# Performance work log

Hardware: AMD Instinct MI355X
Metric: run time of the kernel (lower is better)

Reference implementation:

```python
import jax, jax.numpy as jnp
import numpy as np

B, N, K, DEG = 512, 128, 8, 16
NR = 200            # num_rels (padding idx = NR)
INP, SEM, EMB, L = 32, 16, 32, 3
FEAT = INP - SEM
NN = B * N
E = NN * DEG
OUT = L * EMB       # 96


def _gru_cell(x, h, Wih, Whh, bih, bhh):
    gi = x @ Wih.T + bih
    gh = h @ Whh.T + bhh
    ir, iz, i_n = jnp.split(gi, 3, axis=-1)
    hr, hz, hn = jnp.split(gh, 3, axis=-1)
    r = jax.nn.sigmoid(ir + hr)
    z = jax.nn.sigmoid(iz + hz)
    n = jnp.tanh(i_n + r * hn)
    return (1.0 - z) * n + z * h


def _run_gru(xs, h0, Wih, Whh, bih, bhh):
    # xs: [T, batch, in]
    def step(h, x):
        h2 = _gru_cell(x, h, Wih, Whh, bih, bhh)
        return h2, h2
    hT, ys = jax.lax.scan(step, h0, xs)
    return ys, hT


def _forward(feat, out_nei_rels, in_nei_rels, r_label_node, src, dst, etype, rel_labels,
             rel_emb, w_rel2ent_W, w_rel2ent_b, W_msg, W_self, b_gnn, W_rel,
             gru_bias, gru_Wih_f, gru_Whh_f, gru_bih_f, gru_bhh_f,
             gru_Wih_b, gru_Whh_b, gru_bih_b, gru_bhh_b,
             Wo_W, Wo_b, path_Wih, path_Whh, path_bih, path_bhh, fc_W, fc_b):
    # --- init_ent_emb_matrix: neighbor-relation attention vs target relation ---
    out_e = rel_emb[out_nei_rels]                      # [NN,K,INP]
    in_e = rel_emb[in_nei_rels]                        # [NN,K,INP]
    tgt = rel_emb[r_label_node]                        # [NN,INP]
    out_att = jax.nn.softmax(jnp.einsum('nkd,nd->nk', out_e, tgt), axis=1)
    in_att = jax.nn.softmax(jnp.einsum('nkd,nd->nk', in_e, tgt), axis=1)
    out_sem = jnp.einsum('nk,nkd->nd', out_att, out_e)
    in_sem = jnp.einsum('nk,nkd->nd', in_att, in_e)
    sem = jax.nn.sigmoid(jnp.concatenate([out_sem, in_sem], axis=1) @ w_rel2ent_W + w_rel2ent_b)
    h = jnp.concatenate([feat, sem], axis=1)           # [NN,INP]

    # --- RGCN-style relational message passing; repr = concat of layer outputs ---
    r = rel_emb
    deg = jnp.maximum(jax.ops.segment_sum(jnp.ones((E,), h.dtype), dst, NN), 1.0)[:, None]
    reprs = []
    for l in range(L):
        msg = h[src] * r[etype]                        # [E,EMB]  (gather-heavy)
        agg = jax.ops.segment_sum(msg, dst, NN) / deg  # mean aggregation
        h = jax.nn.relu(agg @ W_msg[l] + h @ W_self[l] + b_gnn[l])
        r = r @ W_rel[l]                               # relation stream (padding row stays 0)
        reprs.append(h)
    repr_ = jnp.concatenate(reprs, axis=1)             # [NN,OUT]
    r_emb_out = r                                      # [NR+1,EMB]

    # --- BatchGRU: bidirectional GRU over each graph's node sequence ---
    node = repr_.reshape(B, N, OUT)
    message = jax.nn.relu(node + gru_bias)
    h0 = jnp.max(node, axis=1)                         # per-graph max init hidden
    xs = jnp.swapaxes(message, 0, 1)                   # [N,B,OUT]
    ys_f, _ = _run_gru(xs, h0, gru_Wih_f, gru_Whh_f, gru_bih_f, gru_bhh_f)
    ys_b, _ = _run_gru(xs[::-1], h0, gru_Wih_b, gru_Whh_b, gru_bih_b, gru_bhh_b)
    gru_out = jnp.concatenate([ys_f, ys_b[::-1]], axis=-1)  # [N,B,2*OUT]
    repr2 = jax.nn.relu(jnp.swapaxes(gru_out, 0, 1).reshape(NN, 2 * OUT))
    node_hidden = jax.nn.relu(repr2 @ Wo_W + Wo_b)     # [NN,OUT]

    nh = node_hidden.reshape(B, N, OUT)
    g_out = jnp.mean(nh, axis=1)                       # mean_nodes
    head_embs = nh[:, 0]                               # node id==1 is node 0 of each graph
    tail_embs = nh[:, 1]                               # node id==2 is node 1 of each graph

    # --- nei_rel_path: GRU over (h_r, r_t, t_r) triples, attention aggregation ---
    in_rels = in_nei_rels.reshape(B, N, K)
    heads_rels = in_rels[:, 0]                         # [B,K]
    tails_rels = in_rels[:, 1]                         # [B,K]
    P = K * K
    paths = jnp.stack([
        jnp.repeat(heads_rels, K, axis=1),
        jnp.broadcast_to(rel_labels[:, None], (B, P)),
        jnp.tile(tails_rels, (1, K)),
    ], axis=-1).reshape(B * P, 3)
    pe = r_emb_out[paths]                              # [B*P,3,EMB]
    _, last = _run_gru(jnp.swapaxes(pe, 0, 1), jnp.zeros((B * P, EMB), pe.dtype),
                       path_Wih, path_Whh, path_bih, path_bhh)
    last = last.reshape(B, P, EMB)
    r_lab_e = r_emb_out[rel_labels]                    # [B,EMB]
    atts = jax.nn.softmax(jnp.einsum('bpe,be->bp', last, r_lab_e), axis=1)
    g_p = jnp.einsum('bp,bpe->be', atts, last)         # [B,EMB]

    g_rep = jnp.concatenate([g_out, head_embs, tail_embs, r_lab_e, g_p], axis=1)  # [B,352]
    return g_rep @ fc_W + fc_b                         # [B,1]


def setup_inputs():
    key = jax.random.key(0)
    ks = jax.random.split(key, 40)
    idx = iter(range(40))
    def nk():
        return ks[next(idx)]
    def _p(shape, scale=0.1):
        return jax.random.normal(nk(), shape, jnp.float32) * scale

    feat = jax.random.normal(nk(), (NN, FEAT), jnp.float32)
    out_nei_rels = jax.random.randint(nk(), (NN, K), 0, NR)
    in_nei_rels = jax.random.randint(nk(), (NN, K), 0, NR)
    rel_labels = jax.random.randint(nk(), (B,), 0, NR)
    r_label_node = jnp.repeat(rel_labels, N)
    gid = jnp.arange(E) // (N * DEG)                   # edges stay within their graph
    src = gid * N + jax.random.randint(nk(), (E,), 0, N)
    dst = gid * N + jax.random.randint(nk(), (E,), 0, N)
    etype = jax.random.randint(nk(), (E,), 0, NR)
    rel_emb = jax.random.normal(nk(), (NR + 1, INP), jnp.float32) * 0.5
    rel_emb = rel_emb.at[NR].set(0.0)                  # padding_idx row

    return {
        'feat': feat, 'out_nei_rels': out_nei_rels, 'in_nei_rels': in_nei_rels,
        'r_label_node': r_label_node, 'src': src, 'dst': dst, 'etype': etype,
        'rel_labels': rel_labels, 'rel_emb': rel_emb,
        'w_rel2ent_W': _p((2 * INP, SEM)), 'w_rel2ent_b': _p((SEM,)),
        'W_msg': _p((L, EMB, EMB)), 'W_self': _p((L, EMB, EMB)),
        'b_gnn': _p((L, EMB)), 'W_rel': _p((L, INP, INP)),
        'gru_bias': _p((OUT,)),
        'gru_Wih_f': _p((3 * OUT, OUT)), 'gru_Whh_f': _p((3 * OUT, OUT)),
        'gru_bih_f': _p((3 * OUT,)), 'gru_bhh_f': _p((3 * OUT,)),
        'gru_Wih_b': _p((3 * OUT, OUT)), 'gru_Whh_b': _p((3 * OUT, OUT)),
        'gru_bih_b': _p((3 * OUT,)), 'gru_bhh_b': _p((3 * OUT,)),
        'Wo_W': _p((2 * OUT, OUT)), 'Wo_b': _p((OUT,)),
        'path_Wih': _p((3 * EMB, EMB)), 'path_Whh': _p((3 * EMB, EMB)),
        'path_bih': _p((3 * EMB,)), 'path_bhh': _p((3 * EMB,)),
        'fc_W': _p((3 * OUT + 2 * EMB, 1)), 'fc_b': _p((1,)),
    }


def reference(feat, out_nei_rels, in_nei_rels, r_label_node, src, dst, etype, rel_labels,
              rel_emb, w_rel2ent_W, w_rel2ent_b, W_msg, W_self, b_gnn, W_rel,
              gru_bias, gru_Wih_f, gru_Whh_f, gru_bih_f, gru_bhh_f,
              gru_Wih_b, gru_Whh_b, gru_bih_b, gru_bhh_b,
              Wo_W, Wo_b, path_Wih, path_Whh, path_bih, path_bhh, fc_W, fc_b):
    return _forward(feat, out_nei_rels, in_nei_rels, r_label_node, src, dst, etype, rel_labels,
                    rel_emb, w_rel2ent_W, w_rel2ent_b, W_msg, W_self, b_gnn, W_rel,
                    gru_bias, gru_Wih_f, gru_Whh_f, gru_bih_f, gru_bhh_f,
                    gru_Wih_b, gru_Whh_b, gru_bih_b, gru_bhh_b,
                    Wo_W, Wo_b, path_Wih, path_Whh, path_bih, path_bhh, fc_W, fc_b)
```

## Files before the change

### kernel.cpp

```cpp
#include <hip/hip_runtime.h>
#include <math.h>

#define BB 512
#define NT 128
#define NREL 201
#define NNODE (BB*NT)
#define NEDGE (NNODE*16)

typedef float f32x4 __attribute__((ext_vector_type(4)));
typedef __attribute__((ext_vector_type(8))) short bf16x8;

__device__ __forceinline__ float sigm(float x) { return 1.f/(1.f + __expf(-x)); }

__device__ __forceinline__ unsigned short f2bf(float f) {
  unsigned u; __builtin_memcpy(&u, &f, 4);
  unsigned r = u + 0x7fffu + ((u >> 16) & 1u);
  return (unsigned short)(r >> 16);
}

__global__ __launch_bounds__(96) void k_rel2(const float* __restrict__ rel_emb,
                                             const float* __restrict__ W_rel,
                                             const float* __restrict__ pWih,
                                             const float* __restrict__ pbih,
                                             float* __restrict__ r123,
                                             float* __restrict__ XI) {
  __shared__ float ra[32], rb[32];
  int r = blockIdx.x, tid = threadIdx.x;
  if (tid < 32) ra[tid] = rel_emb[r*32 + tid];
  __syncthreads();
  if (tid < 32) {
    float s = 0.f;
    #pragma unroll
    for (int d = 0; d < 32; ++d) s += ra[d]*W_rel[d*32 + tid];
    rb[tid] = s; r123[0*NREL*32 + r*32 + tid] = s;
  }
  __syncthreads();
  if (tid < 32) {
    float s = 0.f;
    #pragma unroll
    for (int d = 0; d < 32; ++d) s += rb[d]*W_rel[1024 + d*32 + tid];
    ra[tid] = s; r123[1*NREL*32 + r*32 + tid] = s;
  }
  __syncthreads();
  if (tid < 32) {
    float s = 0.f;
    #pragma unroll
    for (int d = 0; d < 32; ++d) s += ra[d]*W_rel[2048 + d*32 + tid];
    rb[tid] = s; r123[2*NREL*32 + r*32 + tid] = s;
  }
  __syncthreads();
  float s = pbih[tid];
  #pragma unroll
  for (int d = 0; d < 32; ++d) s += rb[d]*pWih[tid*32 + d];
  XI[r*96 + tid] = s;
}

__global__ __launch_bounds__(256) void k_wt1(const float* __restrict__ Wih_f,
                                             const float* __restrict__ Wih_b,
                                             const float* __restrict__ bih_f,
                                             const float* __restrict__ bih_b,
                                             const float* __restrict__ Wo_W,
                                             unsigned short* __restrict__ WT1bt,
                                             unsigned short* __restrict__ WoBt,
                                             float* __restrict__ bcat) {
  int i = blockIdx.x*256 + threadIdx.x;
  if (i < 576*96) {
    int j = i / 96;
    float v = (j < 288) ? Wih_f[i] : Wih_b[i - 288*96];
    WT1bt[i] = f2bf(v);
  }
  if (i < 96*192) {
    int j = i / 192, k = i - j*192;
    WoBt[i] = f2bf(Wo_W[k*96 + j]);
  }
  if (i < 576) bcat[i] = (i < 288) ? bih_f[i] : bih_b[i-288];
}

__device__ __forceinline__ void sem_att(const float* __restrict__ rel_emb,
                                        const int rels[8], const float tgt[32],
                                        float out[32]) {
  float dots[8]; float mx = -1e30f;
  #pragma unroll
  for (int k = 0; k < 8; ++k) {
    const float4* er = (const float4*)(rel_emb + rels[k]*32);
    float s = 0.f;
    #pragma unroll
    for (int q = 0; q < 8; ++q) {
      float4 v = er[q];
      s += v.x*tgt[4*q+0] + v.y*tgt[4*q+1] + v.z*tgt[4*q+2] + v.w*tgt[4*q+3];
    }
    dots[k] = s; mx = fmaxf(mx, s);
  }
  float den = 0.f;
  #pragma unroll
  for (int k = 0; k < 8; ++k) { float e = __expf(dots[k]-mx); dots[k] = e; den += e; }
  float inv = 1.f/den;
  #pragma unroll
  for (int d = 0; d < 32; ++d) out[d] = 0.f;
  #pragma unroll
  for (int k = 0; k < 8; ++k) {
    const float4* er = (const float4*)(rel_emb + rels[k]*32);
    float a = dots[k]*inv;
    #pragma unroll
    for (int q = 0; q < 8; ++q) {
      float4 v = er[q];
      out[4*q+0] += a*v.x; out[4*q+1] += a*v.y; out[4*q+2] += a*v.z; out[4*q+3] += a*v.w;
    }
  }
}

__global__ __launch_bounds__(256) void k_sem(
    const float* __restrict__ feat, const int* __restrict__ out_rels,
    const int* __restrict__ in_rels, const int* __restrict__ r_label_node,
    const float* __restrict__ rel_emb, const float* __restrict__ W,
    const float* __restrict__ bias, float* __restrict__ hin) {
  int n = blockIdx.x*256 + threadIdx.x;
  float tgt[32];
  {
    const float4* tr = (const float4*)(rel_emb + r_label_node[n]*32);
    #pragma unroll
    for (int q = 0; q < 8; ++q) {
      float4 v = tr[q];
      tgt[4*q+0]=v.x; tgt[4*q+1]=v.y; tgt[4*q+2]=v.z; tgt[4*q+3]=v.w;
    }
  }
  int ro[8], ri[8];
  #pragma unroll
  for (int k = 0; k < 8; ++k) { ro[k] = out_rels[n*8+k]; ri[k] = in_rels[n*8+k]; }
  float osem[32], isem[32];
  sem_att(rel_emb, ro, tgt, osem);
  sem_att(rel_emb, ri, tgt, isem);
  const float4* fr = (const float4*)(feat + (size_t)n*16);
  float4* ho = (float4*)(hin + (size_t)n*32);
  #pragma unroll
  for (int q = 0; q < 4; ++q) ho[q] = fr[q];
  #pragma unroll
  for (int j = 0; j < 16; ++j) {
    float s = bias[j];
    #pragma unroll
    for (int d = 0; d < 32; ++d) s += osem[d]*W[d*16+j] + isem[d]*W[(32+d)*16+j];
    hin[(size_t)n*32 + 16 + j] = sigm(s);
  }
}

__global__ __launch_bounds__(512) void k_gnn3(
    const float* __restrict__ hin, const float* __restrict__ rel_emb,
    const float* __restrict__ r123,
    const int* __restrict__ src, const int* __restrict__ dst, const int* __restrict__ etype,
    const float* __restrict__ W_msg, const float* __restrict__ W_self,
    const float* __restrict__ b_gnn,
    float* __restrict__ AT, float* __restrict__ ghid0) {
  __shared__ __align__(16) float hl[NT*36];
  __shared__ __align__(16) float hnew[NT*33];
  __shared__ float rl[NREL*32];
  __shared__ unsigned short eidx[2048];
  __shared__ float scratch[16][32];
  __shared__ int cnt[128], fill[128], scanv[128], rowstart[129];
  int g = blockIdx.x;
  int tid = threadIdx.x;
  int d = tid & 31, grp = tid >> 5;

  for (int i = tid; i < NT*32; i += 512) {
    int row = i >> 5, col = i & 31;
    hl[row*36 + col] = hin[(size_t)(g*NT + row)*32 + col];
  }
  if (tid < 128) { cnt[tid] = 0; fill[tid] = 0; }
  __syncthreads();
  for (int i = tid; i < 2048; i += 512)
    atomicAdd(&cnt[dst[g*2048 + i] - g*NT], 1);
  __syncthreads();
  if (tid < 128) scanv[tid] = cnt[tid];
  __syncthreads();
  #pragma unroll
  for (int off = 1; off < 128; off <<= 1) {
    int v = 0;
    if (tid < 128 && tid >= off) v = scanv[tid - off];
    __syncthreads();
    if (tid < 128) scanv[tid] += v;
    __syncthreads();
  }
  if (tid < 128) { rowstart[tid+1] = scanv[tid]; if (tid == 0) rowstart[0] = 0; }
  __syncthreads();
  for (int i = tid; i < 2048; i += 512) {
    int e = g*2048 + i;
    int dl = dst[e] - g*NT;
    int slot = rowstart[dl] + atomicAdd(&fill[dl], 1);
    eidx[slot] = (unsigned short)(((src[e] - g*NT) << 8) | etype[e]);
  }

  for (int l = 0; l < 3; ++l) {
    const float* rsrc = (l == 0) ? rel_emb : (r123 + (size_t)(l-1)*NREL*32);
    for (int i = tid; i < NREL*32; i += 512) rl[i] = rsrc[i];
    float wm[32], ws[32];
    #pragma unroll
    for (int dd = 0; dd < 32; ++dd) {
      wm[dd] = W_msg[l*1024 + dd*32 + d];
      ws[dd] = W_self[l*1024 + dd*32 + d];
    }
    float bj = b_gnn[l*32 + d];
    __syncthreads();
    for (int k2 = 0; k2 < 8; ++k2) {
      int n = grp + k2*16;
      int e0 = rowstart[n], e1 = rowstart[n+1];
      float acc = 0.f;
      for (int e = e0; e < e1; ++e) {
        int pk = eidx[e];
        acc += hl[(pk >> 8)*36 + d] * rl[(pk & 255)*32 + d];
      }
      scratch[grp][d] = acc;
      float invd = 1.f / (float)((e1 - e0) > 0 ? (e1 - e0) : 1);
      float sa = 0.f, sh = 0.f;
      #pragma unroll
      for (int dd = 0; dd < 32; ++dd) {
        sa += scratch[grp][dd]*wm[dd];
        sh += hl[n*36 + dd]*ws[dd];
      }
      hnew[n*33 + d] = fmaxf(bj + invd*sa + sh, 0.f);
    }
    __syncthreads();
    for (int i = tid; i < NT*32; i += 512) {
      int row = i >> 5, col = i & 31;
      hl[row*36 + col] = hnew[row*33 + col];
    }
    #pragma unroll
    for (int pass = 0; pass < 8; ++pass) {
      int col = (pass << 2) + (tid >> 7);
      int row = tid & 127;
      AT[(size_t)(l*32 + col)*NNODE + g*NT + row] = hnew[row*33 + col];
    }
    {
      float m = -1e30f;
      #pragma unroll
      for (int k2 = 0; k2 < 8; ++k2) m = fmaxf(m, hnew[(grp + k2*16)*33 + d]);
      scratch[grp][d] = m;
    }
    __syncthreads();
    if (tid < 32) {
      float m = -1e30f;
      #pragma unroll
      for (int p2 = 0; p2 < 16; ++p2) m = fmaxf(m, scratch[p2][tid]);
      ghid0[g*96 + l*32 + tid] = m;
    }
    __syncthreads();
  }
}

__global__ __launch_bounds__(256) void k_gemm1m(
    const float* __restrict__ AT, const float* __restrict__ gbias,
    const unsigned short* __restrict__ WT1bt, const float* __restrict__ bcat,
    float* __restrict__ GI) {
  __shared__ unsigned short As[128*104];
  int m0 = blockIdx.x * 128;
  int tid = threadIdx.x;
  for (int i = tid; i < 96*32; i += 256) {
    int r = i >> 5, c4 = i & 31;
    float4 v = *(const float4*)&AT[(size_t)r*NNODE + m0 + c4*4];
    float b = gbias[r];
    As[(c4*4+0)*104 + r] = f2bf(fmaxf(v.x+b,0.f));
    As[(c4*4+1)*104 + r] = f2bf(fmaxf(v.y+b,0.f));
    As[(c4*4+2)*104 + r] = f2bf(fmaxf(v.z+b,0.f));
    As[(c4*4+3)*104 + r] = f2bf(fmaxf(v.w+b,0.f));
  }
  __syncthreads();
  int w = tid >> 6, l = tid & 63;
  int lr = l & 15, lh = l >> 4;
  bf16x8 afr[2][3];
  #pragma unroll
  for (int tm = 0; tm < 2; ++tm)
    #pragma unroll
    for (int kc = 0; kc < 3; ++kc)
      afr[tm][kc] = *(const bf16x8*)&As[((w*2+tm)*16 + lr)*104 + kc*32 + lh*8];
  for (int nb = 0; nb < 9; ++nb) {
    int n0 = nb*64;
    #pragma unroll
    for (int tn = 0; tn < 4; ++tn) {
      int col = n0 + tn*16 + lr;
      const unsigned short* bp = WT1bt + (size_t)col*96 + lh*8;
      bf16x8 b0 = *(const bf16x8*)(bp);
      bf16x8 b1 = *(const bf16x8*)(bp + 32);
      bf16x8 b2 = *(const bf16x8*)(bp + 64);
      float bb = bcat[col];
      #pragma unroll
      for (int tm = 0; tm < 2; ++tm) {
        f32x4 acc = {bb, bb, bb, bb};
        acc = __builtin_amdgcn_mfma_f32_16x16x32_bf16(afr[tm][0], b0, acc, 0, 0, 0);
        acc = __builtin_amdgcn_mfma_f32_16x16x32_bf16(afr[tm][1], b1, acc, 0, 0, 0);
        acc = __builtin_amdgcn_mfma_f32_16x16x32_bf16(afr[tm][2], b2, acc, 0, 0, 0);
        int rbase = m0 + (w*2+tm)*16 + lh*4;
        #pragma unroll
        for (int r = 0; r < 4; ++r)
          __builtin_nontemporal_store(acc[r], &GI[(size_t)(rbase + r)*576 + col]);
      }
    }
  }
}

#define PIN4(v) asm volatile("" : "+v"(v.x), "+v"(v.y), "+v"(v.z), "+v"(v.w))
#define DOT16(acc, W0,W1,W2,W3, X0,X1,X2,X3) \
  acc += W0.x*X0.x + W0.y*X0.y + W0.z*X0.z + W0.w*X0.w \
       + W1.x*X1.x + W1.y*X1.y + W1.z*X1.z + W1.w*X1.w \
       + W2.x*X2.x + W2.y*X2.y + W2.z*X2.z + W2.w*X2.w \
       + W3.x*X3.x + W3.y*X3.y + W3.z*X3.z + W3.w*X3.w

__global__ __launch_bounds__(576, 1) void k_gru(
    const float* __restrict__ Whh_f, const float* __restrict__ bhh_f,
    const float* __restrict__ Whh_b, const float* __restrict__ bhh_b,
    const float* __restrict__ GI, const float* __restrict__ ghid0,
    float* __restrict__ AT2) {
  __shared__ __align__(16) float h_lds[4][96];
  __shared__ float part[4][288][9];
  int bx = blockIdx.x;
  int dir = bx >> 7;
  int gbase = (bx & 127) * 4;
  int tid = threadIdx.x;
  int c = tid % 96;
  int p = tid / 96;
  bool fin = (tid < 384);
  int s = p;

  const float* Whh = dir ? Whh_b : Whh_f;
  const float4* wr0 = (const float4*)(Whh + (size_t)c*96 + p*16);
  const float4* wr1 = (const float4*)(Whh + (size_t)(96+c)*96 + p*16);
  const float4* wr2 = (const float4*)(Whh + (size_t)(192+c)*96 + p*16);
  float4 wa0=wr0[0], wa1=wr0[1], wa2=wr0[2], wa3=wr0[3];
  float4 wb0=wr1[0], wb1=wr1[1], wb2=wr1[2], wb3=wr1[3];
  float4 wc0=wr2[0], wc1=wr2[1], wc2=wr2[2], wc3=wr2[3];

  float bh0=0.f, bh1=0.f, bh2=0.f;
  float gi0=0.f, gi1=0.f, gi2=0.f;
  if (fin) {
    const float* bhh = dir ? bhh_b : bhh_f;
    bh0 = bhh[c]; bh1 = bhh[96+c]; bh2 = bhh[192+c];
    h_lds[s][c] = ghid0[(gbase+s)*96 + c];
    int pos0 = dir ? 127 : 0;
    const float* g = GI + (size_t)((gbase+s)*128 + pos0)*576 + dir*288;
    gi0 = g[c]; gi1 = g[96+c]; gi2 = g[192+c];
  }
  __syncthreads();
  for (int t = 0; t < 128; ++t) {
    PIN4(wa0); PIN4(wa1); PIN4(wa2); PIN4(wa3);
    PIN4(wb0); PIN4(wb1); PIN4(wb2); PIN4(wb3);
    PIN4(wc0); PIN4(wc1); PIN4(wc2); PIN4(wc3);
    int pos = dir ? (127-t) : t;
    float gn0=0.f, gn1=0.f, gn2=0.f;
    if (fin && t < 127) {
      int posn = dir ? (126-t) : (t+1);
      const float* g = GI + (size_t)((gbase+s)*128 + posn)*576 + dir*288;
      gn0 = g[c]; gn1 = g[96+c]; gn2 = g[192+c];
    }
    #pragma unroll
    for (int s4 = 0; s4 < 4; ++s4) {
      const float4* hh = (const float4*)&h_lds[s4][p*16];
      float4 x0=hh[0], x1=hh[1], x2=hh[2], x3=hh[3];
      float q0=0.f, q1=0.f, q2=0.f;
      DOT16(q0, wa0,wa1,wa2,wa3, x0,x1,x2,x3);
      DOT16(q1, wb0,wb1,wb2,wb3, x0,x1,x2,x3);
      DOT16(q2, wc0,wc1,wc2,wc3, x0,x1,x2,x3);
      part[s4][c][p]     = q0;
      part[s4][96+c][p]  = q1;
      part[s4][192+c][p] = q2;
    }
    __syncthreads();
    if (fin) {
      const float* pr = part[s][c];
      const float* pz = part[s][96+c];
      const float* pn = part[s][192+c];
      float ghr = pr[0]+pr[1]+pr[2]+pr[3]+pr[4]+pr[5] + bh0;
      float ghz = pz[0]+pz[1]+pz[2]+pz[3]+pz[4]+pz[5] + bh1;
      float ghn = pn[0]+pn[1]+pn[2]+pn[3]+pn[4]+pn[5] + bh2;
      float r  = sigm(gi0 + ghr);
      float z  = sigm(gi1 + ghz);
      float nn = tanhf(gi2 + r*ghn);
      float hv = (1.f - z)*nn + z*h_lds[s][c];
      h_lds[s][c] = hv;
      AT2[(size_t)(dir*96 + c)*NNODE + (gbase+s)*128 + pos] = fmaxf(hv, 0.f);
      gi0 = gn0; gi1 = gn1; gi2 = gn2;
    }
    __syncthreads();
  }
}

__global__ __launch_bounds__(384) void k_gemm2m(
    const float* __restrict__ AT2, const unsigned short* __restrict__ WoBt,
    const float* __restrict__ Wob, float* __restrict__ goutb,
    float* __restrict__ headb, float* __restrict__ tailb) {
  __shared__ unsigned short As[64*104];
  int m0 = blockIdx.x * 64;
  int g = m0 >> 7;
  int tid = threadIdx.x;
  int w = tid / 64, l = tid & 63;
  int lr = l & 15, lh = l >> 4;
  int col = w*16 + lr;
  float bb = Wob[col];
  f32x4 acc[4];
  #pragma unroll
  for (int mt = 0; mt < 4; ++mt) acc[mt] = (f32x4){bb, bb, bb, bb};
  for (int kc = 0; kc < 2; ++kc) {
    if (kc) __syncthreads();
    for (int i = tid; i < 1536; i += 384) {
      int r = i >> 4, c4 = i & 15;
      float4 v = *(const float4*)&AT2[(size_t)(kc*96 + r)*NNODE + m0 + c4*4];
      As[(c4*4+0)*104 + r] = f2bf(v.x);
      As[(c4*4+1)*104 + r] = f2bf(v.y);
      As[(c4*4+2)*104 + r] = f2bf(v.z);
      As[(c4*4+3)*104 + r] = f2bf(v.w);
    }
    __syncthreads();
    const unsigned short* bp = WoBt + (size_t)col*192 + kc*96 + lh*8;
    bf16x8 b0 = *(const bf16x8*)(bp);
    bf16x8 b1 = *(const bf16x8*)(bp + 32);
    bf16x8 b2 = *(const bf16x8*)(bp + 64);
    #pragma unroll
    for (int mt = 0; mt < 4; ++mt) {
      const unsigned short* ap = &As[(mt*16 + lr)*104 + lh*8];
      bf16x8 a0 = *(const bf16x8*)(ap);
      bf16x8 a1 = *(const bf16x8*)(ap + 32);
      bf16x8 a2 = *(const bf16x8*)(ap + 64);
      acc[mt] = __builtin_amdgcn_mfma_f32_16x16x32_bf16(a0, b0, acc[mt], 0, 0, 0);
      acc[mt] = __builtin_amdgcn_mfma_f32_16x16x32_bf16(a1, b1, acc[mt], 0, 0, 0);
      acc[mt] = __builtin_amdgcn_mfma_f32_16x16x32_bf16(a2, b2, acc[mt], 0, 0, 0);
    }
  }
  float colsum = 0.f;
  bool hb = ((m0 & 127) == 0) && (lh == 0);
  #pragma unroll
  for (int mt = 0; mt < 4; ++mt) {
    #pragma unroll
    for (int r = 0; r < 4; ++r) {
      float v = fmaxf(acc[mt][r], 0.f);
      colsum += v;
      if (hb && mt == 0) {
        if (r == 0) headb[g*96 + col] = v;
        if (r == 1) tailb[g*96 + col] = v;
      }
    }
  }
  colsum += __shfl_xor(colsum, 16);
  colsum += __shfl_xor(colsum, 32);
  if (lh == 0) atomicAdd(&goutb[g*96 + col], colsum);
}

__global__ __launch_bounds__(128) void k_path(
    const float* __restrict__ XI, const int* __restrict__ in_rels,
    const int* __restrict__ labels, const float* __restrict__ pWhh,
    const float* __restrict__ pbhh, float* __restrict__ last) {
  __shared__ __align__(16) float wsh[96*32];
  __shared__ float bsh[96];
  __shared__ float hbuf[128*33];
  int tid = threadIdx.x;
  for (int i = tid; i < 96*32; i += 128) wsh[i] = pWhh[i];
  if (tid < 96) bsh[tid] = pbhh[tid];
  int p = blockIdx.x*128 + tid;
  int b = p >> 6, pp = p & 63;
  int rid0 = in_rels[b*1024 + (pp >> 3)];
  int rid1 = labels[b];
  int rid2 = in_rels[b*1024 + 8 + (pp & 7)];
  __syncthreads();
  float* hs = &hbuf[tid*33];
  {
    const float* xi = XI + rid0*96;
    #pragma unroll
    for (int gg = 0; gg < 32; ++gg) {
      float r = sigm(xi[gg] + bsh[gg]);
      float z = sigm(xi[32+gg] + bsh[32+gg]);
      float nn = tanhf(xi[64+gg] + r*bsh[64+gg]);
      hs[gg] = (1.f - z)*nn;
    }
  }
  float4 h4[8];
  #pragma unroll
  for (int q = 0; q < 8; ++q) h4[q] = make_float4(hs[4*q], hs[4*q+1], hs[4*q+2], hs[4*q+3]);
  for (int s = 0; s < 2; ++s) {
    const float* xi = XI + (s == 0 ? rid1 : rid2)*96;
    for (int gg = 0; gg < 32; ++gg) {
      float ar = bsh[gg], az = bsh[32+gg], an = bsh[64+gg];
      const float4* wr = (const float4*)&wsh[gg*32];
      const float4* wz = (const float4*)&wsh[(32+gg)*32];
      const float4* wn = (const float4*)&wsh[(64+gg)*32];
      #pragma unroll
      for (int q = 0; q < 8; ++q) {
        float4 hv = h4[q]; float4 w;
        w = wr[q]; ar += hv.x*w.x + hv.y*w.y + hv.z*w.z + hv.w*w.w;
        w = wz[q]; az += hv.x*w.x + hv.y*w.y + hv.z*w.z + hv.w*w.w;
        w = wn[q]; an += hv.x*w.x + hv.y*w.y + hv.z*w.z + hv.w*w.w;
      }
      float r = sigm(xi[gg] + ar);
      float z = sigm(xi[32+gg] + az);
      float nn = tanhf(xi[64+gg] + r*an);
      hs[gg] = (1.f - z)*nn + z*hs[gg];
    }
    #pragma unroll
    for (int q = 0; q < 8; ++q) h4[q] = make_float4(hs[4*q], hs[4*q+1], hs[4*q+2], hs[4*q+3]);
  }
  float* lp = last + (size_t)p*32;
  #pragma unroll
  for (int d = 0; d < 32; ++d) lp[d] = hs[d];
}

__global__ __launch_bounds__(64) void k_final(
    const float* __restrict__ last, const float* __restrict__ r3,
    const int* __restrict__ labels, const float* __restrict__ goutb,
    const float* __restrict__ headb, const float* __restrict__ tailb,
    const float* __restrict__ fcW, const float* __restrict__ fcb,
    float* __restrict__ out) {
  __shared__ float red[64*33];
  __shared__ float gpl[32];
  int b = blockIdx.x, lane = threadIdx.x;
  const float* rl = r3 + labels[b]*32;
  float l32[32];
  {
    const float4* lr = (const float4*)(last + (size_t)(b*64 + lane)*32);
    #pragma unroll
    for (int q = 0; q < 8; ++q) {
      float4 v = lr[q];
      l32[4*q+0]=v.x; l32[4*q+1]=v.y; l32[4*q+2]=v.z; l32[4*q+3]=v.w;
    }
  }
  float s = 0.f;
  #pragma unroll
  for (int d = 0; d < 32; ++d) s += l32[d]*rl[d];
  float mx = s;
  #pragma unroll
  for (int off = 32; off > 0; off >>= 1) mx = fmaxf(mx, __shfl_xor(mx, off));
  float e = __expf(s - mx);
  float den = e;
  #pragma unroll
  for (int off = 32; off > 0; off >>= 1) den += __shfl_xor(den, off);
  float att = e / den;
  #pragma unroll
  for (int d = 0; d < 32; ++d) red[lane*33 + d] = att*l32[d];
  __syncthreads();
  if (lane < 32) {
    float gp = 0.f;
    for (int p2 = 0; p2 < 64; ++p2) gp += red[p2*33 + lane];
    gpl[lane] = gp;
  }
  __syncthreads();
  float acc = 0.f;
  for (int i = lane; i < 352; i += 64) {
    float v;
    if (i < 96)       v = goutb[b*96 + i] * 0.0078125f;
    else if (i < 192) v = headb[b*96 + (i-96)];
    else if (i < 288) v = tailb[b*96 + (i-192)];
    else if (i < 320) v = rl[i-288];
    else              v = gpl[i-320];
    acc += v*fcW[i];
  }
  #pragma unroll
  for (int off = 32; off > 0; off >>= 1) acc += __shfl_xor(acc, off);
  if (lane == 0) out[b] = acc + fcb[0];
}

extern "C" void kernel_launch(void* const* d_in, const int* in_sizes, int n_in,
                              void* d_out, int out_size, void* d_ws, size_t ws_size,
                              hipStream_t stream) {
  const float* feat       = (const float*)d_in[0];
  const int*   out_rels   = (const int*)d_in[1];
  const int*   in_rels    = (const int*)d_in[2];
  const int*   r_label_nd = (const int*)d_in[3];
  const int*   src        = (const int*)d_in[4];
  const int*   dst        = (const int*)d_in[5];
  const int*   etype      = (const int*)d_in[6];
  const int*   rel_labels = (const int*)d_in[7];
  const float* rel_emb    = (const float*)d_in[8];
  const float* w2e_W      = (const float*)d_in[9];
  const float* w2e_b      = (const float*)d_in[10];
  const float* W_msg      = (const float*)d_in[11];
  const float* W_self     = (const float*)d_in[12];
  const float* b_gnn      = (const float*)d_in[13];
  const float* W_rel      = (const float*)d_in[14];
  const float* gru_bias   = (const float*)d_in[15];
  const float* Wih_f      = (const float*)d_in[16];
  const float* Whh_f      = (const float*)d_in[17];
  const float* bih_f      = (const float*)d_in[18];
  const float* bhh_f      = (const float*)d_in[19];
  const float* Wih_b      = (const float*)d_in[20];
  const float* Whh_b      = (const float*)d_in[21];
  const float* bih_b      = (const float*)d_in[22];
  const float* bhh_b      = (const float*)d_in[23];
  const float* Wo_W       = (const float*)d_in[24];
  const float* Wo_b       = (const float*)d_in[25];
  const float* pWih       = (const float*)d_in[26];
  const float* pWhh       = (const float*)d_in[27];
  const float* pbih       = (const float*)d_in[28];
  const float* pbhh       = (const float*)d_in[29];
  const float* fcW        = (const float*)d_in[30];
  const float* fcb        = (const float*)d_in[31];
  float* out = (float*)d_out;

  float* p = (float*)d_ws;
  float* hin   = p; p += (size_t)NNODE*32;
  float* R1    = p; p += (size_t)NNODE*192;
  float* AT    = R1;
  float* AT2   = R1;
  float* GI    = p; p += (size_t)NNODE*576 + 16;
  float* r123  = p; p += 3*NREL*32;
  unsigned short* WT1bt = (unsigned short*)p; p += (576*96)/2;
  unsigned short* WoBt  = (unsigned short*)p; p += (96*192)/2;
  float* bcat  = p; p += 576;
  float* XI    = p; p += NREL*96;
  float* ghid0 = p; p += BB*96;
  float* goutb = p; p += BB*96;
  float* headb = p; p += BB*96;
  float* tailb = p; p += BB*96;
  float* lastb = p; p += (size_t)BB*64*32;

  hipMemsetAsync(goutb, 0, BB*96*sizeof(float), stream);
  k_rel2<<<NREL, 96, 0, stream>>>(rel_emb, W_rel, pWih, pbih, r123, XI);
  k_wt1<<<(576*96+255)/256, 256, 0, stream>>>(Wih_f, Wih_b, bih_f, bih_b, Wo_W,
                                              WT1bt, WoBt, bcat);
  k_sem<<<NNODE/256, 256, 0, stream>>>(feat, out_rels, in_rels, r_label_nd,
                                       rel_emb, w2e_W, w2e_b, hin);
  k_gnn3<<<BB, 512, 0, stream>>>(hin, rel_emb, r123, src, dst, etype,
                                 W_msg, W_self, b_gnn, AT, ghid0);
  k_gemm1m<<<512, 256, 0, stream>>>(AT, gru_bias, WT1bt, bcat, GI);
  k_gru<<<256, 576, 0, stream>>>(Whh_f, bhh_f, Whh_b, bhh_b, GI, ghid0, AT2);
  k_gemm2m<<<1024, 384, 0, stream>>>(AT2, WoBt, Wo_b, goutb, headb, tailb);
  k_path<<<256, 128, 0, stream>>>(XI, in_rels, rel_labels, pWhh, pbhh, lastb);
  k_final<<<BB, 64, 0, stream>>>(lastb, r123 + 2*NREL*32, rel_labels,
                                 goutb, headb, tailb, fcW, fcb, out);
}
```

Before: 461.5 us.

## Fuse semantic attention into GNN kernel and path GRU into sequence GRU launch

The per-node relation-attention init is moved into the GNN block, reading relation embeddings from shared memory and writing h directly to LDS. This removes the hin global round trip and one launch. The path GRU runs as extra blocks of the bidirectional GRU kernel, sharing LDS through a union, so it overlaps with the latency-bound recurrence. In exchange, only 128 of 512 threads do the attention work inside the GNN block, and launch_bounds changes to 2 blocks per CU for the GRU, which may cost register pressure.

```diff
diff --git a/kernel.cpp b/kernel.cpp
--- a/kernel.cpp
+++ b/kernel.cpp
@@ -76,13 +76,13 @@
   if (i < 576) bcat[i] = (i < 288) ? bih_f[i] : bih_b[i-288];
 }
 
-__device__ __forceinline__ void sem_att(const float* __restrict__ rel_emb,
-                                        const int rels[8], const float tgt[32],
-                                        float out[32]) {
+__device__ __forceinline__ void sem_att_l(const float* __restrict__ rl,
+                                          const int rels[8], const float tgt[32],
+                                          float out[32]) {
   float dots[8]; float mx = -1e30f;
   #pragma unroll
   for (int k = 0; k < 8; ++k) {
-    const float4* er = (const float4*)(rel_emb + rels[k]*32);
+    const float4* er = (const float4*)&rl[rels[k]*32];
     float s = 0.f;
     #pragma unroll
     for (int q = 0; q < 8; ++q) {
@@ -99,7 +99,7 @@
   for (int d = 0; d < 32; ++d) out[d] = 0.f;
   #pragma unroll
   for (int k = 0; k < 8; ++k) {
-    const float4* er = (const float4*)(rel_emb + rels[k]*32);
+    const float4* er = (const float4*)&rl[rels[k]*32];
     float a = dots[k]*inv;
     #pragma unroll
     for (int q = 0; q < 8; ++q) {
@@ -109,50 +109,18 @@
   }
 }
 
-__global__ __launch_bounds__(256) void k_sem(
+__global__ __launch_bounds__(512) void k_gnn3(
     const float* __restrict__ feat, const int* __restrict__ out_rels,
     const int* __restrict__ in_rels, const int* __restrict__ r_label_node,
-    const float* __restrict__ rel_emb, const float* __restrict__ W,
-    const float* __restrict__ bias, float* __restrict__ hin) {
-  int n = blockIdx.x*256 + threadIdx.x;
-  float tgt[32];
-  {
-    const float4* tr = (const float4*)(rel_emb + r_label_node[n]*32);
-    #pragma unroll
-    for (int q = 0; q < 8; ++q) {
-      float4 v = tr[q];
-      tgt[4*q+0]=v.x; tgt[4*q+1]=v.y; tgt[4*q+2]=v.z; tgt[4*q+3]=v.w;
-    }
-  }
-  int ro[8], ri[8];
-  #pragma unroll
-  for (int k = 0; k < 8; ++k) { ro[k] = out_rels[n*8+k]; ri[k] = in_rels[n*8+k]; }
-  float osem[32], isem[32];
-  sem_att(rel_emb, ro, tgt, osem);
-  sem_att(rel_emb, ri, tgt, isem);
-  const float4* fr = (const float4*)(feat + (size_t)n*16);
-  float4* ho = (float4*)(hin + (size_t)n*32);
-  #pragma unroll
-  for (int q = 0; q < 4; ++q) ho[q] = fr[q];
-  #pragma unroll
-  for (int j = 0; j < 16; ++j) {
-    float s = bias[j];
-    #pragma unroll
-    for (int d = 0; d < 32; ++d) s += osem[d]*W[d*16+j] + isem[d]*W[(32+d)*16+j];
-    hin[(size_t)n*32 + 16 + j] = sigm(s);
-  }
-}
-
-__global__ __launch_bounds__(512) void k_gnn3(
-    const float* __restrict__ hin, const float* __restrict__ rel_emb,
-    const float* __restrict__ r123,
+    const float* __restrict__ w2e_W, const float* __restrict__ w2e_b,
+    const float* __restrict__ rel_emb, const float* __restrict__ r123,
     const int* __restrict__ src, const int* __restrict__ dst, const int* __restrict__ etype,
     const float* __restrict__ W_msg, const float* __restrict__ W_self,
     const float* __restrict__ b_gnn,
     float* __restrict__ AT, float* __restrict__ ghid0) {
   __shared__ __align__(16) float hl[NT*36];
   __shared__ __align__(16) float hnew[NT*33];
-  __shared__ float rl[NREL*32];
+  __shared__ __align__(16) float rl[NREL*32];
   __shared__ unsigned short eidx[2048];
   __shared__ float scratch[16][32];
   __shared__ int cnt[128], fill[128], scanv[128], rowstart[129];
@@ -160,10 +128,7 @@
   int tid = threadIdx.x;
   int d = tid & 31, grp = tid >> 5;
 
-  for (int i = tid; i < NT*32; i += 512) {
-    int row = i >> 5, col = i & 31;
-    hl[row*36 + col] = hin[(size_t)(g*NT + row)*32 + col];
-  }
+  for (int i = tid; i < NREL*32; i += 512) rl[i] = rel_emb[i];
   if (tid < 128) { cnt[tid] = 0; fill[tid] = 0; }
   __syncthreads();
   for (int i = tid; i < 2048; i += 512)
@@ -187,10 +152,44 @@
     int slot = rowstart[dl] + atomicAdd(&fill[dl], 1);
     eidx[slot] = (unsigned short)(((src[e] - g*NT) << 8) | etype[e]);
   }
+  if (tid < 128) {
+    int n = g*NT + tid;
+    float tgt[32];
+    {
+      const float4* tr = (const float4*)&rl[r_label_node[n]*32];
+      #pragma unroll
+      for (int q = 0; q < 8; ++q) {
+        float4 v = tr[q];
+        tgt[4*q+0]=v.x; tgt[4*q+1]=v.y; tgt[4*q+2]=v.z; tgt[4*q+3]=v.w;
+      }
+    }
+    int ro[8], ri[8];
+    #pragma unroll
+    for (int k = 0; k < 8; ++k) { ro[k] = out_rels[n*8+k]; ri[k] = in_rels[n*8+k]; }
+    float osem[32], isem[32];
+    sem_att_l(rl, ro, tgt, osem);
+    sem_att_l(rl, ri, tgt, isem);
+    const float4* fr = (const float4*)(feat + (size_t)n*16);
+    #pragma unroll
+    for (int q = 0; q < 4; ++q) {
+      float4 v = fr[q];
+      hl[tid*36 + 4*q+0] = v.x; hl[tid*36 + 4*q+1] = v.y;
+      hl[tid*36 + 4*q+2] = v.z; hl[tid*36 + 4*q+3] = v.w;
+    }
+    #pragma unroll
+    for (int j = 0; j < 16; ++j) {
+      float s = w2e_b[j];
+      #pragma unroll
+      for (int dd = 0; dd < 32; ++dd) s += osem[dd]*w2e_W[dd*16+j] + isem[dd]*w2e_W[(32+dd)*16+j];
+      hl[tid*36 + 16 + j] = sigm(s);
+    }
+  }
 
   for (int l = 0; l < 3; ++l) {
-    const float* rsrc = (l == 0) ? rel_emb : (r123 + (size_t)(l-1)*NREL*32);
-    for (int i = tid; i < NREL*32; i += 512) rl[i] = rsrc[i];
+    if (l > 0) {
+      const float* rsrc = r123 + (size_t)(l-1)*NREL*32;
+      for (int i = tid; i < NREL*32; i += 512) rl[i] = rsrc[i];
+    }
     float wm[32], ws[32];
     #pragma unroll
     for (int dd = 0; dd < 32; ++dd) {
@@ -302,81 +301,143 @@
        + W2.x*X2.x + W2.y*X2.y + W2.z*X2.z + W2.w*X2.w \
        + W3.x*X3.x + W3.y*X3.y + W3.z*X3.z + W3.w*X3.w
 
-__global__ __launch_bounds__(576, 1) void k_gru(
+union GPShared {
+  struct { float h_lds[4][96]; float part[4][288][9]; } g;
+  struct { float wsh[96*32]; float bsh[96]; float hbuf[128*33]; } p;
+};
+
+__global__ __launch_bounds__(576, 2) void k_grup(
     const float* __restrict__ Whh_f, const float* __restrict__ bhh_f,
     const float* __restrict__ Whh_b, const float* __restrict__ bhh_b,
     const float* __restrict__ GI, const float* __restrict__ ghid0,
-    float* __restrict__ AT2) {
-  __shared__ __align__(16) float h_lds[4][96];
-  __shared__ float part[4][288][9];
+    float* __restrict__ AT2,
+    const float* __restrict__ XI, const int* __restrict__ in_rels,
+    const int* __restrict__ labels, const float* __restrict__ pWhh,
+    const float* __restrict__ pbhh, float* __restrict__ last) {
+  __shared__ GPShared sm;
   int bx = blockIdx.x;
-  int dir = bx >> 7;
-  int gbase = (bx & 127) * 4;
   int tid = threadIdx.x;
-  int c = tid % 96;
-  int p = tid / 96;
-  bool fin = (tid < 384);
-  int s = p;
-
-  const float* Whh = dir ? Whh_b : Whh_f;
-  const float4* wr0 = (const float4*)(Whh + (size_t)c*96 + p*16);
-  const float4* wr1 = (const float4*)(Whh + (size_t)(96+c)*96 + p*16);
-  const float4* wr2 = (const float4*)(Whh + (size_t)(192+c)*96 + p*16);
-  float4 wa0=wr0[0], wa1=wr0[1], wa2=wr0[2], wa3=wr0[3];
-  float4 wb0=wr1[0], wb1=wr1[1], wb2=wr1[2], wb3=wr1[3];
-  float4 wc0=wr2[0], wc1=wr2[1], wc2=wr2[2], wc3=wr2[3];
-
-  float bh0=0.f, bh1=0.f, bh2=0.f;
-  float gi0=0.f, gi1=0.f, gi2=0.f;
-  if (fin) {
-    const float* bhh = dir ? bhh_b : bhh_f;
-    bh0 = bhh[c]; bh1 = bhh[96+c]; bh2 = bhh[192+c];
-    h_lds[s][c] = ghid0[(gbase+s)*96 + c];
-    int pos0 = dir ? 127 : 0;
-    const float* g = GI + (size_t)((gbase+s)*128 + pos0)*576 + dir*288;
-    gi0 = g[c]; gi1 = g[96+c]; gi2 = g[192+c];
-  }
-  __syncthreads();
-  for (int t = 0; t < 128; ++t) {
-    PIN4(wa0); PIN4(wa1); PIN4(wa2); PIN4(wa3);
-    PIN4(wb0); PIN4(wb1); PIN4(wb2); PIN4(wb3);
-    PIN4(wc0); PIN4(wc1); PIN4(wc2); PIN4(wc3);
-    int pos = dir ? (127-t) : t;
-    float gn0=0.f, gn1=0.f, gn2=0.f;
-    if (fin && t < 127) {
-      int posn = dir ? (126-t) : (t+1);
-      const float* g = GI + (size_t)((gbase+s)*128 + posn)*576 + dir*288;
-      gn0 = g[c]; gn1 = g[96+c]; gn2 = g[192+c];
-    }
-    #pragma unroll
-    for (int s4 = 0; s4 < 4; ++s4) {
-      const float4* hh = (const float4*)&h_lds[s4][p*16];
-      float4 x0=hh[0], x1=hh[1], x2=hh[2], x3=hh[3];
-      float q0=0.f, q1=0.f, q2=0.f;
-      DOT16(q0, wa0,wa1,wa2,wa3, x0,x1,x2,x3);
-      DOT16(q1, wb0,wb1,wb2,wb3, x0,x1,x2,x3);
-      DOT16(q2, wc0,wc1,wc2,wc3, x0,x1,x2,x3);
-      part[s4][c][p]     = q0;
-      part[s4][96+c][p]  = q1;
-      part[s4][192+c][p] = q2;
-    }
-    __syncthreads();
+  if (bx < 256) {
+    float (*h_lds)[96] = sm.g.h_lds;
+    float (*part)[288][9] = sm.g.part;
+    int dir = bx >> 7;
+    int gbase = (bx & 127) * 4;
+    int c = tid % 96;
+    int p = tid / 96;
+    bool fin = (tid < 384);
+    int s = p;
+    const float* Whh = dir ? Whh_b : Whh_f;
+    const float4* wr0 = (const float4*)(Whh + (size_t)c*96 + p*16);
+    const float4* wr1 = (const float4*)(Whh + (size_t)(96+c)*96 + p*16);
+    const float4* wr2 = (const float4*)(Whh + (size_t)(192+c)*96 + p*16);
+    float4 wa0=wr0[0], wa1=wr0[1], wa2=wr0[2], wa3=wr0[3];
+    float4 wb0=wr1[0], wb1=wr1[1], wb2=wr1[2], wb3=wr1[3];
+    float4 wc0=wr2[0], wc1=wr2[1], wc2=wr2[2], wc3=wr2[3];
+    float bh0=0.f, bh1=0.f, bh2=0.f;
+    float gi0=0.f, gi1=0.f, gi2=0.f;
     if (fin) {
-      const float* pr = part[s][c];
-      const float* pz = part[s][96+c];
-      const float* pn = part[s][192+c];
-      float ghr = pr[0]+pr[1]+pr[2]+pr[3]+pr[4]+pr[5] + bh0;
-      float ghz = pz[0]+pz[1]+pz[2]+pz[3]+pz[4]+pz[5] + bh1;
-      float ghn = pn[0]+pn[1]+pn[2]+pn[3]+pn[4]+pn[5] + bh2;
-      float r  = sigm(gi0 + ghr);
-      float z  = sigm(gi1 + ghz);
-      float nn = tanhf(gi2 + r*ghn);
-      float hv = (1.f - z)*nn + z*h_lds[s][c];
-      h_lds[s][c] = hv;
-      AT2[(size_t)(dir*96 + c)*NNODE + (gbase+s)*128 + pos] = fmaxf(hv, 0.f);
-      gi0 = gn0; gi1 = gn1; gi2 = gn2;
-    }
-    __syncthreads();
+      const float* bhh = dir ? bhh_b : bhh_f;
+      bh0 = bhh[c]; bh1 = bhh[96+c]; bh2 = bhh[192+c];
+      h_lds[s][c] = ghid0[(gbase+s)*96 + c];
+      int pos0 = dir ? 127 : 0;
+      const float* gg = GI + (size_t)((gbase+s)*128 + pos0)*576 + dir*288;
+      gi0 = gg[c]; gi1 = gg[96+c]; gi2 = gg[192+c];
+    }
+    __syncthreads();
+    for (int t = 0; t < 128; ++t) {
+      PIN4(wa0); PIN4(wa1); PIN4(wa2); PIN4(wa3);
+      PIN4(wb0); PIN4(wb1); PIN4(wb2); PIN4(wb3);
+      PIN4(wc0); PIN4(wc1); PIN4(wc2); PIN4(wc3);
+      int pos = dir ? (127-t) : t;
+      float gn0=0.f, gn1=0.f, gn2=0.f;
+      if (fin && t < 127) {
+        int posn = dir ? (126-t) : (t+1);
+        const float* gg = GI + (size_t)((gbase+s)*128 + posn)*576 + dir*288;
+        gn0 = gg[c]; gn1 = gg[96+c]; gn2 = gg[192+c];
+      }
+      #pragma unroll
+      for (int s4 = 0; s4 < 4; ++s4) {
+        const float4* hh = (const float4*)&h_lds[s4][p*16];
+        float4 x0=hh[0], x1=hh[1], x2=hh[2], x3=hh[3];
+        float q0=0.f, q1=0.f, q2=0.f;
+        DOT16(q0, wa0,wa1,wa2,wa3, x0,x1,x2,x3);
+        DOT16(q1, wb0,wb1,wb2,wb3, x0,x1,x2,x3);
+        DOT16(q2, wc0,wc1,wc2,wc3, x0,x1,x2,x3);
+        part[s4][c][p]     = q0;
+        part[s4][96+c][p]  = q1;
+        part[s4][192+c][p] = q2;
+      }
+      __syncthreads();
+      if (fin) {
+        const float* pr = part[s][c];
+        const float* pz = part[s][96+c];
+        const float* pn = part[s][192+c];
+        float ghr = pr[0]+pr[1]+pr[2]+pr[3]+pr[4]+pr[5] + bh0;
+        float ghz = pz[0]+pz[1]+pz[2]+pz[3]+pz[4]+pz[5] + bh1;
+        float ghn = pn[0]+pn[1]+pn[2]+pn[3]+pn[4]+pn[5] + bh2;
+        float r  = sigm(gi0 + ghr);
+        float z  = sigm(gi1 + ghz);
+        float nn = tanhf(gi2 + r*ghn);
+        float hv = (1.f - z)*nn + z*h_lds[s][c];
+        h_lds[s][c] = hv;
+        AT2[(size_t)(dir*96 + c)*NNODE + (gbase+s)*128 + pos] = fmaxf(hv, 0.f);
+        gi0 = gn0; gi1 = gn1; gi2 = gn2;
+      }
+      __syncthreads();
+    }
+  } else {
+    float* wsh = sm.p.wsh;
+    float* bsh = sm.p.bsh;
+    float* hbuf = sm.p.hbuf;
+    for (int i = tid; i < 96*32; i += 576) wsh[i] = pWhh[i];
+    if (tid < 96) bsh[tid] = pbhh[tid];
+    __syncthreads();
+    if (tid < 128) {
+      int pth = (bx - 256)*128 + tid;
+      int b = pth >> 6, pp = pth & 63;
+      int rid0 = in_rels[b*1024 + (pp >> 3)];
+      int rid1 = labels[b];
+      int rid2 = in_rels[b*1024 + 8 + (pp & 7)];
+      float* hs = &hbuf[tid*33];
+      {
+        const float* xi = XI + rid0*96;
+        #pragma unroll
+        for (int gg = 0; gg < 32; ++gg) {
+          float r = sigm(xi[gg] + bsh[gg]);
+          float z = sigm(xi[32+gg] + bsh[32+gg]);
+          float nn = tanhf(xi[64+gg] + r*bsh[64+gg]);
+          hs[gg] = (1.f - z)*nn;
+        }
+      }
+      float4 h4[8];
+      #pragma unroll
+      for (int q = 0; q < 8; ++q) h4[q] = make_float4(hs[4*q], hs[4*q+1], hs[4*q+2], hs[4*q+3]);
+      for (int s = 0; s < 2; ++s) {
+        const float* xi = XI + (s == 0 ? rid1 : rid2)*96;
+        for (int gg = 0; gg < 32; ++gg) {
+          float ar = bsh[gg], az = bsh[32+gg], an = bsh[64+gg];
+          const float4* wr = (const float4*)&wsh[gg*32];
+          const float4* wz = (const float4*)&wsh[(32+gg)*32];
+          const float4* wn = (const float4*)&wsh[(64+gg)*32];
+          #pragma unroll
+          for (int q = 0; q < 8; ++q) {
+            float4 hv = h4[q]; float4 w;
+            w = wr[q]; ar += hv.x*w.x + hv.y*w.y + hv.z*w.z + hv.w*w.w;
+            w = wz[q]; az += hv.x*w.x + hv.y*w.y + hv.z*w.z + hv.w*w.w;
+            w = wn[q]; an += hv.x*w.x + hv.y*w.y + hv.z*w.z + hv.w*w.w;
+          }
+          float r = sigm(xi[gg] + ar);
+          float z = sigm(xi[32+gg] + az);
+          float nn = tanhf(xi[64+gg] + r*an);
+          hs[gg] = (1.f - z)*nn + z*hs[gg];
+        }
+        #pragma unroll
+        for (int q = 0; q < 8; ++q) h4[q] = make_float4(hs[4*q], hs[4*q+1], hs[4*q+2], hs[4*q+3]);
+      }
+      float* lp = last + (size_t)pth*32;
+      #pragma unroll
+      for (int dd = 0; dd < 32; ++dd) lp[dd] = hs[dd];
+    }
   }
 }
 
@@ -438,63 +499,6 @@
   colsum += __shfl_xor(colsum, 16);
   colsum += __shfl_xor(colsum, 32);
   if (lh == 0) atomicAdd(&goutb[g*96 + col], colsum);
-}
-
-__global__ __launch_bounds__(128) void k_path(
-    const float* __restrict__ XI, const int* __restrict__ in_rels,
-    const int* __restrict__ labels, const float* __restrict__ pWhh,
-    const float* __restrict__ pbhh, float* __restrict__ last) {
-  __shared__ __align__(16) float wsh[96*32];
-  __shared__ float bsh[96];
-  __shared__ float hbuf[128*33];
-  int tid = threadIdx.x;
-  for (int i = tid; i < 96*32; i += 128) wsh[i] = pWhh[i];
-  if (tid < 96) bsh[tid] = pbhh[tid];
-  int p = blockIdx.x*128 + tid;
-  int b = p >> 6, pp = p & 63;
-  int rid0 = in_rels[b*1024 + (pp >> 3)];
-  int rid1 = labels[b];
-  int rid2 = in_rels[b*1024 + 8 + (pp & 7)];
-  __syncthreads();
-  float* hs = &hbuf[tid*33];
-  {
-    const float* xi = XI + rid0*96;
-    #pragma unroll
-    for (int gg = 0; gg < 32; ++gg) {
-      float r = sigm(xi[gg] + bsh[gg]);
-      float z = sigm(xi[32+gg] + bsh[32+gg]);
-      float nn = tanhf(xi[64+gg] + r*bsh[64+gg]);
-      hs[gg] = (1.f - z)*nn;
-    }
-  }
-  float4 h4[8];
-  #pragma unroll
-  for (int q = 0; q < 8; ++q) h4[q] = make_float4(hs[4*q], hs[4*q+1], hs[4*q+2], hs[4*q+3]);
-  for (int s = 0; s < 2; ++s) {
-    const float* xi = XI + (s == 0 ? rid1 : rid2)*96;
-    for (int gg = 0; gg < 32; ++gg) {
-      float ar = bsh[gg], az = bsh[32+gg], an = bsh[64+gg];
-      const float4* wr = (const float4*)&wsh[gg*32];
-      const float4* wz = (const float4*)&wsh[(32+gg)*32];
-      const float4* wn = (const float4*)&wsh[(64+gg)*32];
-      #pragma unroll
-      for (int q = 0; q < 8; ++q) {
-        float4 hv = h4[q]; float4 w;
-        w = wr[q]; ar += hv.x*w.x + hv.y*w.y + hv.z*w.z + hv.w*w.w;
-        w = wz[q]; az += hv.x*w.x + hv.y*w.y + hv.z*w.z + hv.w*w.w;
-        w = wn[q]; an += hv.x*w.x + hv.y*w.y + hv.z*w.z + hv.w*w.w;
-      }
-      float r = sigm(xi[gg] + ar);
-      float z = sigm(xi[32+gg] + az);
-      float nn = tanhf(xi[64+gg] + r*an);
-      hs[gg] = (1.f - z)*nn + z*hs[gg];
-    }
-    #pragma unroll
-    for (int q = 0; q < 8; ++q) h4[q] = make_float4(hs[4*q], hs[4*q+1], hs[4*q+2], hs[4*q+3]);
-  }
-  float* lp = last + (size_t)p*32;
-  #pragma unroll
-  for (int d = 0; d < 32; ++d) lp[d] = hs[d];
 }
 
 __global__ __launch_bounds__(64) void k_final(
@@ -589,7 +593,6 @@
   float* out = (float*)d_out;
 
   float* p = (float*)d_ws;
-  float* hin   = p; p += (size_t)NNODE*32;
   float* R1    = p; p += (size_t)NNODE*192;
   float* AT    = R1;
   float* AT2   = R1;
@@ -609,14 +612,13 @@
   k_rel2<<<NREL, 96, 0, stream>>>(rel_emb, W_rel, pWih, pbih, r123, XI);
   k_wt1<<<(576*96+255)/256, 256, 0, stream>>>(Wih_f, Wih_b, bih_f, bih_b, Wo_W,
                                               WT1bt, WoBt, bcat);
-  k_sem<<<NNODE/256, 256, 0, stream>>>(feat, out_rels, in_rels, r_label_nd,
-                                       rel_emb, w2e_W, w2e_b, hin);
-  k_gnn3<<<BB, 512, 0, stream>>>(hin, rel_emb, r123, src, dst, etype,
+  k_gnn3<<<BB, 512, 0, stream>>>(feat, out_rels, in_rels, r_label_nd,
+                                 w2e_W, w2e_b, rel_emb, r123, src, dst, etype,
                                  W_msg, W_self, b_gnn, AT, ghid0);
   k_gemm1m<<<512, 256, 0, stream>>>(AT, gru_bias, WT1bt, bcat, GI);
-  k_gru<<<256, 576, 0, stream>>>(Whh_f, bhh_f, Whh_b, bhh_b, GI, ghid0, AT2);
+  k_grup<<<512, 576, 0, stream>>>(Whh_f, bhh_f, Whh_b, bhh_b, GI, ghid0, AT2,
+                                  XI, in_rels, rel_labels, pWhh, pbhh, lastb);
   k_gemm2m<<<1024, 384, 0, stream>>>(AT2, WoBt, Wo_b, goutb, headb, tailb);
-  k_path<<<256, 128, 0, stream>>>(XI, in_rels, rel_labels, pWhh, pbhh, lastb);
   k_final<<<BB, 64, 0, stream>>>(lastb, r123 + 2*NREL*32, rel_labels,
                                  goutb, headb, tailb, fcW, fcb, out);
 }
```

After: 538.0 us. +16.6%, slower.
